# Performance work log

Measured on AMD Instinct MI355X. Metric: run time of the kernel, lower is better.

Reference implementation:

```python
import jax, jax.numpy as jnp
import numpy as np

N_PATCHES = 32
N_POINTS = 2048
N_SIGMA = 1


def setup_inputs() -> dict:
    key = jax.random.key(0)
    pcs = jax.random.normal(key, (8192, N_POINTS, 3), dtype=jnp.float32)
    return {"pcs": pcs}


def reference(pcs):
    B = pcs.shape[0]
    P = N_PATCHES
    n = N_POINTS // P  # points per patch
    x = pcs.reshape(B, P, n, 3)
    means = x.mean(axis=2)                 # [B, P, 3]
    stds = x.std(axis=2, ddof=1)           # [B, P, 3] (torch std is unbiased)
    # all-pairs |mean_i - mean_j| and std_i + std_j, [B, P, P, 3]
    delta = jnp.abs(means[:, :, None, :] - means[:, None, :, :])
    ssum = stds[:, :, None, :] + stds[:, None, :, :]
    rep = jax.nn.relu(ssum * N_SIGMA - delta)
    norms = jnp.sqrt(jnp.sum(rep * rep, axis=-1))  # [B, P, P]
    # original loops over i <= j (diagonal included): upper triangle incl. diag
    mask = jnp.triu(jnp.ones((P, P), dtype=norms.dtype))
    n_pairs = P * (P + 1) // 2
    return jnp.sum(norms * mask) / (n_pairs * B)
```

## Files before the change

kernel.cpp:

```cpp
#include <hip/hip_runtime.h>

#define NPTS 2048
#define NPATCH 32
#define PTS_PER_PATCH 64
#define FLOATS_PER_BATCH (NPTS*3)
#define N_PAIRS 528.0f

__global__ __launch_bounds__(256) void patch_stage1(
    const float* __restrict__ pcs, float* __restrict__ ws) {
  const int b   = blockIdx.x;
  const int tid = threadIdx.x;
  const int p   = tid >> 3;
  const int s   = tid & 7;

  const float4* p4 = (const float4*)(pcs + (size_t)b * FLOATS_PER_BATCH) + 48 * p + s;

  float4 v[6];
#pragma unroll
  for (int k = 0; k < 6; ++k) v[k] = p4[8 * k];

  float L0 = 0.f, L1 = 0.f, L2 = 0.f;
  float Q0 = 0.f, Q1 = 0.f, Q2 = 0.f;

#define ACC(k, a, bb, c)                                          \
  { float x = v[k].x, y = v[k].y, z = v[k].z, w = v[k].w;         \
    L##a += x + w; Q##a += x * x + w * w;                         \
    L##bb += y;    Q##bb += y * y;                                \
    L##c += z;     Q##c += z * z; }
  ACC(0, 0, 1, 2)
  ACC(1, 2, 0, 1)
  ACC(2, 1, 2, 0)
  ACC(3, 0, 1, 2)
  ACC(4, 2, 0, 1)
  ACC(5, 1, 2, 0)
#undef ACC

  float sx, sy, sz, sxx, syy, szz;
  const int s3 = s % 3;
  if (s3 == 0)      { sx = L0; sy = L1; sz = L2; sxx = Q0; syy = Q1; szz = Q2; }
  else if (s3 == 1) { sx = L2; sy = L0; sz = L1; sxx = Q2; syy = Q0; szz = Q1; }
  else              { sx = L1; sy = L2; sz = L0; sxx = Q1; syy = Q2; szz = Q0; }

#pragma unroll
  for (int off = 4; off >= 1; off >>= 1) {
    sx  += __shfl_down(sx,  off, 8);
    sy  += __shfl_down(sy,  off, 8);
    sz  += __shfl_down(sz,  off, 8);
    sxx += __shfl_down(sxx, off, 8);
    syy += __shfl_down(syy, off, 8);
    szz += __shfl_down(szz, off, 8);
  }

  __shared__ float smean[NPATCH][4];
  __shared__ float sstd[NPATCH][4];

  if (s == 0) {
    const float inv_n = 1.0f / PTS_PER_PATCH;
    const float inv_nm1 = 1.0f / (PTS_PER_PATCH - 1);
    smean[p][0] = sx * inv_n; smean[p][1] = sy * inv_n; smean[p][2] = sz * inv_n;
    sstd[p][0] = sqrtf(fmaxf((sxx - sx * sx * inv_n) * inv_nm1, 0.f));
    sstd[p][1] = sqrtf(fmaxf((syy - sy * sy * inv_n) * inv_nm1, 0.f));
    sstd[p][2] = sqrtf(fmaxf((szz - sz * sz * inv_n) * inv_nm1, 0.f));
  }
  __syncthreads();

  float acc = 0.f;
#pragma unroll
  for (int r = 0; r < 4; ++r) {
    const int q = tid + 256 * r;
    const int i = q >> 5;
    const int j = q & 31;
    if (i <= j) {
      float rx = fmaxf((sstd[i][0] + sstd[j][0]) - fabsf(smean[i][0] - smean[j][0]), 0.f);
      float ry = fmaxf((sstd[i][1] + sstd[j][1]) - fabsf(smean[i][1] - smean[j][1]), 0.f);
      float rz = fmaxf((sstd[i][2] + sstd[j][2]) - fabsf(smean[i][2] - smean[j][2]), 0.f);
      acc += sqrtf(rx * rx + ry * ry + rz * rz);
    }
  }

#pragma unroll
  for (int off = 32; off >= 1; off >>= 1) acc += __shfl_down(acc, off);
  __shared__ float wpart[4];
  if ((tid & 63) == 0) wpart[tid >> 6] = acc;
  __syncthreads();
  if (tid == 0) ws[b] = wpart[0] + wpart[1] + wpart[2] + wpart[3];
}

__global__ __launch_bounds__(256) void patch_stage2(
    const float* __restrict__ ws, float* __restrict__ out, int B, float scale) {
  float acc = 0.f;
  for (int i = threadIdx.x; i < B; i += 256) acc += ws[i];
#pragma unroll
  for (int off = 32; off >= 1; off >>= 1) acc += __shfl_down(acc, off);
  __shared__ float wpart[4];
  if ((threadIdx.x & 63) == 0) wpart[threadIdx.x >> 6] = acc;
  __syncthreads();
  if (threadIdx.x == 0) out[0] = (wpart[0] + wpart[1] + wpart[2] + wpart[3]) * scale;
}

extern "C" void kernel_launch(void* const* d_in, const int* in_sizes, int n_in,
                              void* d_out, int out_size, void* d_ws, size_t ws_size,
                              hipStream_t stream) {
  const float* pcs = (const float*)d_in[0];
  float* out = (float*)d_out;
  float* ws  = (float*)d_ws;

  const int B = in_sizes[0] / FLOATS_PER_BATCH;
  const float scale = 1.0f / (N_PAIRS * (float)B);

  patch_stage1<<<B, 256, 0, stream>>>(pcs, ws);
  patch_stage2<<<1, 256, 0, stream>>>(ws, out, B, scale);
}
```

Before: 275.6 us.

## Map one batch per wavefront and compute patch pairs via shuffles

```diff
diff --git a/kernel.cpp b/kernel.cpp
--- a/kernel.cpp
+++ b/kernel.cpp
@@ -2,94 +2,82 @@
 
 #define NPTS 2048
 #define NPATCH 32
-#define PTS_PER_PATCH 64
 #define FLOATS_PER_BATCH (NPTS*3)
 #define N_PAIRS 528.0f
 
 __global__ __launch_bounds__(256) void patch_stage1(
     const float* __restrict__ pcs, float* __restrict__ ws) {
-  const int b   = blockIdx.x;
-  const int tid = threadIdx.x;
-  const int p   = tid >> 3;
-  const int s   = tid & 7;
+  const int tid  = threadIdx.x;
+  const int lane = tid & 63;
+  const int h    = lane & 1;
+  const int b    = blockIdx.x * 4 + (tid >> 6);
 
-  const float4* p4 = (const float4*)(pcs + (size_t)b * FLOATS_PER_BATCH) + 48 * p + s;
+  const float4* p4 = (const float4*)(pcs + (size_t)b * FLOATS_PER_BATCH)
+                     + 48 * (lane >> 1) + h;
 
-  float4 v[6];
+  float4 v[24];
 #pragma unroll
-  for (int k = 0; k < 6; ++k) v[k] = p4[8 * k];
+  for (int j = 0; j < 24; ++j) v[j] = p4[2 * j];
 
   float L0 = 0.f, L1 = 0.f, L2 = 0.f;
   float Q0 = 0.f, Q1 = 0.f, Q2 = 0.f;
 
-#define ACC(k, a, bb, c)                                          \
-  { float x = v[k].x, y = v[k].y, z = v[k].z, w = v[k].w;         \
-    L##a += x + w; Q##a += x * x + w * w;                         \
-    L##bb += y;    Q##bb += y * y;                                \
+#define ACC(j, a, bb, c)                                         \
+  { float x = v[j].x, y = v[j].y, z = v[j].z, w = v[j].w;        \
+    L##a += x + w; Q##a += x * x + w * w;                        \
+    L##bb += y;    Q##bb += y * y;                               \
     L##c += z;     Q##c += z * z; }
-  ACC(0, 0, 1, 2)
-  ACC(1, 2, 0, 1)
-  ACC(2, 1, 2, 0)
-  ACC(3, 0, 1, 2)
-  ACC(4, 2, 0, 1)
-  ACC(5, 1, 2, 0)
+  ACC(0,0,1,2)  ACC(1,2,0,1)  ACC(2,1,2,0)
+  ACC(3,0,1,2)  ACC(4,2,0,1)  ACC(5,1,2,0)
+  ACC(6,0,1,2)  ACC(7,2,0,1)  ACC(8,1,2,0)
+  ACC(9,0,1,2)  ACC(10,2,0,1) ACC(11,1,2,0)
+  ACC(12,0,1,2) ACC(13,2,0,1) ACC(14,1,2,0)
+  ACC(15,0,1,2) ACC(16,2,0,1) ACC(17,1,2,0)
+  ACC(18,0,1,2) ACC(19,2,0,1) ACC(20,1,2,0)
+  ACC(21,0,1,2) ACC(22,2,0,1) ACC(23,1,2,0)
 #undef ACC
 
   float sx, sy, sz, sxx, syy, szz;
-  const int s3 = s % 3;
-  if (s3 == 0)      { sx = L0; sy = L1; sz = L2; sxx = Q0; syy = Q1; szz = Q2; }
-  else if (s3 == 1) { sx = L2; sy = L0; sz = L1; sxx = Q2; syy = Q0; szz = Q1; }
-  else              { sx = L1; sy = L2; sz = L0; sxx = Q1; syy = Q2; szz = Q0; }
+  if (h == 0) { sx = L0; sy = L1; sz = L2; sxx = Q0; syy = Q1; szz = Q2; }
+  else        { sx = L2; sy = L0; sz = L1; sxx = Q2; syy = Q0; szz = Q1; }
 
-#pragma unroll
-  for (int off = 4; off >= 1; off >>= 1) {
-    sx  += __shfl_down(sx,  off, 8);
-    sy  += __shfl_down(sy,  off, 8);
-    sz  += __shfl_down(sz,  off, 8);
-    sxx += __shfl_down(sxx, off, 8);
-    syy += __shfl_down(syy, off, 8);
-    szz += __shfl_down(szz, off, 8);
-  }
+  sx  += __shfl_xor(sx,  1);
+  sy  += __shfl_xor(sy,  1);
+  sz  += __shfl_xor(sz,  1);
+  sxx += __shfl_xor(sxx, 1);
+  syy += __shfl_xor(syy, 1);
+  szz += __shfl_xor(szz, 1);
 
-  __shared__ float smean[NPATCH][4];
-  __shared__ float sstd[NPATCH][4];
-
-  if (s == 0) {
-    const float inv_n = 1.0f / PTS_PER_PATCH;
-    const float inv_nm1 = 1.0f / (PTS_PER_PATCH - 1);
-    smean[p][0] = sx * inv_n; smean[p][1] = sy * inv_n; smean[p][2] = sz * inv_n;
-    sstd[p][0] = sqrtf(fmaxf((sxx - sx * sx * inv_n) * inv_nm1, 0.f));
-    sstd[p][1] = sqrtf(fmaxf((syy - sy * sy * inv_n) * inv_nm1, 0.f));
-    sstd[p][2] = sqrtf(fmaxf((szz - sz * sz * inv_n) * inv_nm1, 0.f));
-  }
-  __syncthreads();
+  const float inv_n = 1.0f / 64.0f, inv_nm1 = 1.0f / 63.0f;
+  const float mx = sx * inv_n, my = sy * inv_n, mz = sz * inv_n;
+  const float tx = sqrtf(fmaxf((sxx - sx * sx * inv_n) * inv_nm1, 0.f));
+  const float ty = sqrtf(fmaxf((syy - sy * sy * inv_n) * inv_nm1, 0.f));
+  const float tz = sqrtf(fmaxf((szz - sz * sz * inv_n) * inv_nm1, 0.f));
 
   float acc = 0.f;
+  const int sbase = lane + 32 * h;
 #pragma unroll
-  for (int r = 0; r < 4; ++r) {
-    const int q = tid + 256 * r;
-    const int i = q >> 5;
-    const int j = q & 31;
-    if (i <= j) {
-      float rx = fmaxf((sstd[i][0] + sstd[j][0]) - fabsf(smean[i][0] - smean[j][0]), 0.f);
-      float ry = fmaxf((sstd[i][1] + sstd[j][1]) - fabsf(smean[i][1] - smean[j][1]), 0.f);
-      float rz = fmaxf((sstd[i][2] + sstd[j][2]) - fabsf(smean[i][2] - smean[j][2]), 0.f);
-      acc += sqrtf(rx * rx + ry * ry + rz * rz);
-    }
+  for (int rr = 0; rr < 16; ++rr) {
+    const int src = (sbase + 2 * rr) & 63;
+    const float qmx = __shfl(mx, src), qmy = __shfl(my, src), qmz = __shfl(mz, src);
+    const float qtx = __shfl(tx, src), qty = __shfl(ty, src), qtz = __shfl(tz, src);
+    const float rx = fmaxf((tx + qtx) - fabsf(mx - qmx), 0.f);
+    const float ry = fmaxf((ty + qty) - fabsf(my - qmy), 0.f);
+    const float rz = fmaxf((tz + qtz) - fabsf(mz - qmz), 0.f);
+    const float nrm = sqrtf(rx * rx + ry * ry + rz * rz);
+    acc += ((rr == 0) & (h == 0)) ? 2.0f * nrm : nrm;
   }
+  acc *= 0.5f;
 
 #pragma unroll
   for (int off = 32; off >= 1; off >>= 1) acc += __shfl_down(acc, off);
-  __shared__ float wpart[4];
-  if ((tid & 63) == 0) wpart[tid >> 6] = acc;
-  __syncthreads();
-  if (tid == 0) ws[b] = wpart[0] + wpart[1] + wpart[2] + wpart[3];
+  if (lane == 0) ws[b] = acc;
 }
 
 __global__ __launch_bounds__(256) void patch_stage2(
-    const float* __restrict__ ws, float* __restrict__ out, int B, float scale) {
+    const float* __restrict__ ws, float* __restrict__ out, int n, float scale) {
   float acc = 0.f;
-  for (int i = threadIdx.x; i < B; i += 256) acc += ws[i];
+  for (int i = threadIdx.x; i < n; i += 256) acc += ws[i];
 #pragma unroll
   for (int off = 32; off >= 1; off >>= 1) acc += __shfl_down(acc, off);
   __shared__ float wpart[4];
@@ -108,6 +96,6 @@
   const int B = in_sizes[0] / FLOATS_PER_BATCH;
   const float scale = 1.0f / (N_PAIRS * (float)B);
 
-  patch_stage1<<<B, 256, 0, stream>>>(pcs, ws);
+  patch_stage1<<<B / 4, 256, 0, stream>>>(pcs, ws);
   patch_stage2<<<1, 256, 0, stream>>>(ws, out, B, scale);
 }
```

Measured after the change: 280.0 us. No clear change (+1.6%).
